# Kernel optimization log

Hardware: AMD Instinct MI355X
Metric: run time of the kernel (lower is better)

Reference implementation:

```python
import jax, jax.numpy as jnp
import numpy as np

B, S, HID = 2, 2048, 3072
H, KV, D = 16, 8, 256
EPS = 1e-6
SCALE = D ** -0.5  # query_pre_attn_scalar is None -> head_dim**-0.5
NEG = -1e9


def setup_inputs() -> dict:
    key = jax.random.key(0)
    ks = jax.random.split(key, 7)
    hidden_states = jax.random.normal(ks[0], (B, S, HID), jnp.float32)
    # rotary tables: freqs_cis = exp(i * pos * theta_j), theta_j = 10000^(-2j/D)
    pos = jnp.arange(S, dtype=jnp.float32)
    inv_freq = 1.0 / (10000.0 ** (jnp.arange(0, D, 2, dtype=jnp.float32) / D))  # [D/2]
    ang = pos[:, None] * inv_freq[None, :]  # [S, D/2]
    freqs_cos = jnp.cos(ang)
    freqs_sin = jnp.sin(ang)
    # additive causal mask [1,1,S,S]
    causal = jnp.tril(jnp.ones((S, S), dtype=bool))
    mask = jnp.where(causal, 0.0, NEG).astype(jnp.float32)[None, None]
    q_w = jax.random.normal(ks[1], (HID, H * D), jnp.float32) * 0.02
    k_w = jax.random.normal(ks[2], (HID, KV * D), jnp.float32) * 0.02
    v_w = jax.random.normal(ks[3], (HID, KV * D), jnp.float32) * 0.02
    o_w = jax.random.normal(ks[4], (H * D, HID), jnp.float32) * 0.02
    qnorm_w = jax.random.normal(ks[5], (D,), jnp.float32) * 0.1
    knorm_w = jax.random.normal(ks[6], (D,), jnp.float32) * 0.1
    return dict(hidden_states=hidden_states, freqs_cos=freqs_cos, freqs_sin=freqs_sin,
                mask=mask, q_w=q_w, k_w=k_w, v_w=v_w, o_w=o_w,
                qnorm_w=qnorm_w, knorm_w=knorm_w)


def rmsnorm(x, w, eps=EPS):
    # RMSNorm with add_unit_offset: x * rsqrt(mean(x^2)+eps) * (1 + w)
    x32 = x.astype(jnp.float32)
    n = x32 * jax.lax.rsqrt(jnp.mean(x32 * x32, axis=-1, keepdims=True) + eps)
    return (n * (1.0 + w.astype(jnp.float32))).astype(x.dtype)


def rope(x, cos, sin):
    # x: [B, S, Hx, D]; complex mult with (x1 + i x2), then concat(real, imag)
    x1, x2 = jnp.split(x, 2, axis=-1)  # each [B,S,Hx,D/2]
    c = cos[None, :, None, :]
    s = sin[None, :, None, :]
    return jnp.concatenate([x1 * c - x2 * s, x1 * s + x2 * c], axis=-1)


def reference(hidden_states, freqs_cos, freqs_sin, mask, q_w, k_w, v_w, o_w, qnorm_w, knorm_w):
    bsz, seqlen = hidden_states.shape[0], hidden_states.shape[1]
    xq = (hidden_states @ q_w).reshape(bsz, seqlen, H, D)
    xk = (hidden_states @ k_w).reshape(bsz, seqlen, KV, D)
    xv = (hidden_states @ v_w).reshape(bsz, seqlen, KV, D)
    # QK-norm (use_qk_norm=True)
    xq = rmsnorm(xq, qnorm_w)
    xk = rmsnorm(xk, knorm_w)
    # rotary embeddings
    xq = rope(xq, freqs_cos, freqs_sin)
    xk = rope(xk, freqs_cos, freqs_sin)
    # GQA: repeat kv heads to match query heads
    rep = H // KV
    xk = jnp.repeat(xk, rep, axis=2)
    xv = jnp.repeat(xv, rep, axis=2)
    q = jnp.transpose(xq, (0, 2, 1, 3)) * SCALE  # [B,H,S,D]
    k = jnp.transpose(xk, (0, 2, 1, 3))
    v = jnp.transpose(xv, (0, 2, 1, 3))
    scores = jnp.einsum('bhqd,bhkd->bhqk', q, k) + mask
    probs = jax.nn.softmax(scores.astype(jnp.float32), axis=-1).astype(q.dtype)
    out = jnp.einsum('bhqk,bhkd->bhqd', probs, v)
    out = jnp.transpose(out, (0, 2, 1, 3)).reshape(bsz, seqlen, H * D)
    return out @ o_w
```

## Files before the change

### kernel.cpp

```cpp
#include <hip/hip_runtime.h>
#include <hip/hip_bf16.h>
#include <cstdint>

#define B_   2
#define S_   2048
#define HID_ 3072
#define H_   16
#define KV_  8
#define D_   256
#define HD_  4096
#define KVD_ 2048
#define QKS_ 8192

constexpr float EPS_   = 1e-6f;
constexpr float SCALE_ = 0.0625f;

typedef unsigned short u16;
typedef __attribute__((ext_vector_type(8))) short bf16x8;
typedef __attribute__((ext_vector_type(4))) float f32x4;

__device__ inline float bf2f(u16 u) { return __uint_as_float(((unsigned int)u) << 16); }
__device__ inline u16 f2bf(float f) {
  unsigned int x = __float_as_uint(f);
  x += 0x7fffu + ((x >> 16) & 1u);
  return (u16)(x >> 16);
}

__device__ inline void gll16(const u16* g, u16* l) {
  __builtin_amdgcn_global_load_lds((const __attribute__((address_space(1))) unsigned int*)g,
                                   (__attribute__((address_space(3))) unsigned int*)l,
                                   16, 0, 0);
}

__global__ void cast_f32_bf16(const float* __restrict__ in, u16* __restrict__ out, int n4) {
  int i = blockIdx.x * blockDim.x + threadIdx.x;
  if (i < n4) {
    float4 v = ((const float4*)in)[i];
    ushort4 o;
    o.x = f2bf(v.x); o.y = f2bf(v.y); o.z = f2bf(v.z); o.w = f2bf(v.w);
    ((ushort4*)out)[i] = o;
  }
}

__global__ void transpose_cast(const float* __restrict__ in, u16* __restrict__ out, int K, int N) {
  __shared__ __align__(16) float tile[64][65];
  int n0 = blockIdx.x * 64, k0 = blockIdx.y * 64;
  int t = threadIdx.x;
  int rr = t >> 4, cc = (t & 15) * 4;
  for (int i = 0; i < 4; i++) {
    float4 v = *(const float4*)(&in[(size_t)(k0 + rr + 16 * i) * N + n0 + cc]);
    tile[rr + 16 * i][cc + 0] = v.x; tile[rr + 16 * i][cc + 1] = v.y;
    tile[rr + 16 * i][cc + 2] = v.z; tile[rr + 16 * i][cc + 3] = v.w;
  }
  __syncthreads();
  for (int i = 0; i < 4; i++) {
    int orow = rr + 16 * i;
    ushort4 o;
    o.x = f2bf(tile[cc + 0][orow]); o.y = f2bf(tile[cc + 1][orow]);
    o.z = f2bf(tile[cc + 2][orow]); o.w = f2bf(tile[cc + 3][orow]);
    *(ushort4*)(&out[(size_t)(n0 + orow) * K + k0 + cc]) = o;
  }
}

__global__ void transpose_v(const u16* __restrict__ in, u16* __restrict__ out) {
  __shared__ __align__(16) u16 tile[64][68];
  int n0 = blockIdx.x * 64, tk0 = blockIdx.y * 64;
  int b = tk0 >> 11, s0 = tk0 & (S_ - 1);
  int t = threadIdx.x;
  int rr = t >> 4, cc = (t & 15) * 4;
  for (int i = 0; i < 4; i++) {
    ushort4 v = *(const ushort4*)(&in[(size_t)(tk0 + rr + 16 * i) * QKS_ + n0 + cc]);
    tile[rr + 16 * i][cc + 0] = v.x; tile[rr + 16 * i][cc + 1] = v.y;
    tile[rr + 16 * i][cc + 2] = v.z; tile[rr + 16 * i][cc + 3] = v.w;
  }
  __syncthreads();
  for (int i = 0; i < 4; i++) {
    int orow = rr + 16 * i;
    ushort4 o;
    o.x = tile[cc + 0][orow]; o.y = tile[cc + 1][orow];
    o.z = tile[cc + 2][orow]; o.w = tile[cc + 3][orow];
    *(ushort4*)(&out[((size_t)b << 22) + (size_t)(n0 + orow) * S_ + s0 + cc]) = o;
  }
}

template <bool OUTF32>
__global__ __launch_bounds__(512, 2) void gemm256(const u16* __restrict__ A,
                                                  const u16* __restrict__ Bt,
                                                  void* __restrict__ Cv, int M, int N, int K) {
  __shared__ __align__(16) u16 As[2][16384];
  __shared__ __align__(16) u16 Bs[2][16384];
  int t = threadIdx.x, lane = t & 63, wave = t >> 6;
  int quad = lane >> 4, l16 = lane & 15;
  int wm = wave >> 2, wn = wave & 3;

  int nwg = gridDim.x * gridDim.y;
  int bid = blockIdx.y * gridDim.x + blockIdx.x;
  int sbid = (bid & 7) * (nwg >> 3) + (bid >> 3);
  int bn = (sbid % gridDim.x) * 256;
  int bm = (sbid / gridDim.x) * 256;

  int srow = lane >> 2;
  int scol8 = ((lane & 3) ^ ((lane >> 3) & 3)) * 8;
  const u16* ap = A + (size_t)(bm + srow) * K + scol8;
  const u16* bp = Bt + (size_t)(bn + srow) * K + scol8;
  int nr = (wave & 1) + ((wave >> 1) << 2);

  auto stA = [&](int sr, int sc, int k0, int bufi) {
    gll16(ap + (size_t)(sr * 16) * K + k0 + sc * 32, &As[bufi][(sr * 2 + sc) * 512]);
  };
  auto stB = [&](int sr, int sc, int k0, int bufi) {
    gll16(bp + (size_t)(sr * 16) * K + k0 + sc * 32, &Bs[bufi][(sr * 2 + sc) * 512]);
  };
  auto stageTile = [&](int kt, int bufi) {
    int k0 = kt * 64;
    stA(wave, 0, k0, bufi); stA(wave, 1, k0, bufi);
    stA(wave + 8, 0, k0, bufi); stA(wave + 8, 1, k0, bufi);
    stB(nr, 0, k0, bufi); stB(nr, 1, k0, bufi);
    stB(nr + 2, 0, k0, bufi); stB(nr + 2, 1, k0, bufi);
  };

  int rsw = l16 * 32 + ((quad ^ ((l16 >> 1) & 3)) * 8);
  auto LDA = [&](int bufi, int i, int ks) {
    return *(const bf16x8*)(&As[bufi][((wm * 8 + i) * 2 + ks) * 512 + rsw]);
  };
  auto LDB = [&](int bufi, int j, int ks) {
    return *(const bf16x8*)(&Bs[bufi][((wn * 4 + j) * 2 + ks) * 512 + rsw]);
  };

  f32x4 acc[8][4] = {};
  int NT = K >> 6;

  stageTile(0, 0);
  stageTile(1, 1);
  asm volatile("s_waitcnt vmcnt(8)" ::: "memory");
  __builtin_amdgcn_s_barrier();
  asm volatile("" ::: "memory");

  bf16x8 A0[4][2], A1[4][2], B01[2][2], B23[2][2];
#pragma unroll
  for (int j = 0; j < 2; j++) { B01[j][0] = LDB(0, j, 0); B01[j][1] = LDB(0, j, 1); }
#pragma unroll
  for (int i = 0; i < 4; i++) { A0[i][0] = LDA(0, i, 0); A0[i][1] = LDA(0, i, 1); }

#pragma unroll 1
  for (int kt = 0; kt < NT; kt++) {
    int cur = kt & 1, nxt = cur ^ 1;

#pragma unroll
    for (int i = 0; i < 4; i++) { A1[i][0] = LDA(cur, i + 4, 0); A1[i][1] = LDA(cur, i + 4, 1); }
    asm volatile("s_waitcnt lgkmcnt(8)" ::: "memory");
#pragma unroll
    for (int i = 0; i < 4; i++)
#pragma unroll
      for (int j = 0; j < 2; j++) {
        acc[i][j] = __builtin_amdgcn_mfma_f32_16x16x32_bf16(A0[i][0], B01[j][0], acc[i][j], 0, 0, 0);
        acc[i][j] = __builtin_amdgcn_mfma_f32_16x16x32_bf16(A0[i][1], B01[j][1], acc[i][j], 0, 0, 0);
      }
#pragma unroll
    for (int j = 0; j < 2; j++) { B23[j][0] = LDB(cur, j + 2, 0); B23[j][1] = LDB(cur, j + 2, 1); }
    asm volatile("s_waitcnt lgkmcnt(4)" ::: "memory");
#pragma unroll
    for (int i = 0; i < 4; i++)
#pragma unroll
      for (int j = 0; j < 2; j++) {
        acc[i + 4][j] = __builtin_amdgcn_mfma_f32_16x16x32_bf16(A1[i][0], B01[j][0], acc[i + 4][j], 0, 0, 0);
        acc[i + 4][j] = __builtin_amdgcn_mfma_f32_16x16x32_bf16(A1[i][1], B01[j][1], acc[i + 4][j], 0, 0, 0);
      }
    asm volatile("s_waitcnt lgkmcnt(0)" ::: "memory");
    asm volatile("s_waitcnt vmcnt(0)" ::: "memory");
    __builtin_amdgcn_s_barrier();
    asm volatile("" ::: "memory");
    if (kt + 2 < NT) stageTile(kt + 2, cur);
    __builtin_amdgcn_s_setprio(1);
#pragma unroll
    for (int i = 0; i < 4; i++)
#pragma unroll
      for (int j = 0; j < 2; j++) {
        acc[i][j + 2] = __builtin_amdgcn_mfma_f32_16x16x32_bf16(A0[i][0], B23[j][0], acc[i][j + 2], 0, 0, 0);
        acc[i][j + 2] = __builtin_amdgcn_mfma_f32_16x16x32_bf16(A0[i][1], B23[j][1], acc[i][j + 2], 0, 0, 0);
      }
    __builtin_amdgcn_s_setprio(0);
    if (kt + 1 < NT) {
#pragma unroll
      for (int j = 0; j < 2; j++) { B01[j][0] = LDB(nxt, j, 0); B01[j][1] = LDB(nxt, j, 1); }
    }
    __builtin_amdgcn_s_setprio(1);
#pragma unroll
    for (int i = 0; i < 4; i++)
#pragma unroll
      for (int j = 0; j < 2; j++) {
        acc[i + 4][j + 2] = __builtin_amdgcn_mfma_f32_16x16x32_bf16(A1[i][0], B23[j][0], acc[i + 4][j + 2], 0, 0, 0);
        acc[i + 4][j + 2] = __builtin_amdgcn_mfma_f32_16x16x32_bf16(A1[i][1], B23[j][1], acc[i + 4][j + 2], 0, 0, 0);
      }
    __builtin_amdgcn_s_setprio(0);
    if (kt + 1 < NT) {
#pragma unroll
      for (int i = 0; i < 4; i++) { A0[i][0] = LDA(nxt, i, 0); A0[i][1] = LDA(nxt, i, 1); }
    }
  }

#pragma unroll
  for (int i = 0; i < 8; i++)
#pragma unroll
    for (int j = 0; j < 4; j++)
#pragma unroll
      for (int r = 0; r < 4; r++) {
        int row = bm + wm * 128 + i * 16 + quad * 4 + r;
        int col = bn + wn * 64 + j * 16 + l16;
        float v = acc[i][j][r];
        if (OUTF32) ((float*)Cv)[(size_t)row * N + col] = v;
        else ((u16*)Cv)[(size_t)row * N + col] = f2bf(v);
      }
}

__global__ void rmsnorm_rope(u16* __restrict__ x, const float* __restrict__ w,
                             const float* __restrict__ fc, const float* __restrict__ fsn,
                             int nh, int stride, float outscale) {
  int token = blockIdx.x;
  int head = blockIdx.y * 4 + (threadIdx.x >> 6);
  if (head >= nh) return;
  int lane = threadIdx.x & 63;
  int s = token & (S_ - 1);
  u16* p = x + (size_t)token * stride + head * D_;
  float v0 = bf2f(p[lane]);
  float v1 = bf2f(p[lane + 64]);
  float v2 = bf2f(p[lane + 128]);
  float v3 = bf2f(p[lane + 192]);
  float ss = v0 * v0 + v1 * v1 + v2 * v2 + v3 * v3;
  for (int off = 32; off; off >>= 1) ss += __shfl_xor(ss, off, 64);
  float rs = rsqrtf(ss * (1.0f / D_) + EPS_);
  float n0 = v0 * rs * (1.0f + w[lane]);
  float n1 = v1 * rs * (1.0f + w[lane + 64]);
  float n2 = v2 * rs * (1.0f + w[lane + 128]);
  float n3 = v3 * rs * (1.0f + w[lane + 192]);
  float c0 = fc[s * 128 + lane], s0 = fsn[s * 128 + lane];
  float c1 = fc[s * 128 + lane + 64], s1 = fsn[s * 128 + lane + 64];
  p[lane]       = f2bf((n0 * c0 - n2 * s0) * outscale);
  p[lane + 128] = f2bf((n0 * s0 + n2 * c0) * outscale);
  p[lane + 64]  = f2bf((n1 * c1 - n3 * s1) * outscale);
  p[lane + 192] = f2bf((n1 * s1 + n3 * c1) * outscale);
}

__global__ __launch_bounds__(256, 3) void flash_attn(const u16* __restrict__ Q,
                                                     const u16* __restrict__ Kb,
                                                     const u16* __restrict__ Vt,
                                                     u16* __restrict__ O) {
  __shared__ __align__(16) u16 Ks[2][8 * 1024];
  __shared__ __align__(16) u16 Vs[8 * 1024];
  int t = threadIdx.x, lane = t & 63, wave = t >> 6;
  int quad = lane >> 4, l16 = lane & 15;
  int h = blockIdx.y, b = blockIdx.z;
  int kvh = h >> 1;

  int swz = ((lane & 3) ^ ((lane >> 2) & 3)) * 8;
  int rswz = (quad ^ (l16 & 3)) * 8;
  const u16* kst = Kb + (size_t)(b * S_ + (lane >> 2)) * QKS_ + kvh * D_ + wave * 64 + swz;
  const u16* vst = Vt + ((size_t)b << 22) + (size_t)(kvh * D_ + wave * 64 + (lane >> 2)) * S_ + swz;

  auto stageK = [&](int kt, int bufi) {
    u16* kdst = &Ks[bufi][wave * 2048];
    const u16* ksrc = kst + (size_t)(kt * 32) * QKS_;
#pragma unroll
    for (int c2 = 0; c2 < 2; c2++)
#pragma unroll
      for (int r = 0; r < 2; r++)
        gll16(ksrc + (size_t)(r * 16) * QKS_ + c2 * 32, kdst + c2 * 1024 + r * 512);
  };
  auto stageV = [&](int kt) {
    u16* vdst = &Vs[wave * 2048];
#pragma unroll
    for (int c = 0; c < 4; c++)
      gll16(vst + (size_t)(c * 16) * S_ + kt * 32, vdst + c * 512);
  };

#pragma unroll 1
  for (int half = 0; half < 2; half++) {
    int qb = (half == 0) ? (31 - (int)blockIdx.x) * 64 : (int)blockIdx.x * 64;
    int qw = qb + wave * 16;

    bf16x8 qf[8];
    const u16* qp = Q + ((size_t)(b * S_) + qw + l16) * QKS_ + h * D_;
#pragma unroll
    for (int c = 0; c < 8; c++) qf[c] = *(const bf16x8*)(qp + c * 32 + quad * 8);

    f32x4 o_acc[16] = {};
    float m_s = -3e38f, l_s = 0.f;

    int nkt = (qb + 64) >> 5;
    stageK(0, 0);
    stageV(0);
#pragma unroll 1
    for (int kt = 0; kt < nkt; kt++) {
      int cur = kt & 1;
      asm volatile("s_waitcnt vmcnt(4)" ::: "memory");
      __builtin_amdgcn_s_barrier();
      asm volatile("" ::: "memory");
      if (kt + 1 < nkt) stageK(kt + 1, cur ^ 1);

      f32x4 sc0 = {}, sc1 = {};
#pragma unroll
      for (int c = 0; c < 8; c++) {
        bf16x8 k0 = *(const bf16x8*)(&Ks[cur][c * 1024 + l16 * 32 + rswz]);
        bf16x8 k1 = *(const bf16x8*)(&Ks[cur][c * 1024 + (l16 + 16) * 32 + rswz]);
        sc0 = __builtin_amdgcn_mfma_f32_16x16x32_bf16(k0, qf[c], sc0, 0, 0, 0);
        sc1 = __builtin_amdgcn_mfma_f32_16x16x32_bf16(k1, qf[c], sc1, 0, 0, 0);
      }

      int qg = qw + l16;
      int kbase = kt * 32 + quad * 4;
      float p0[4], p1[4];
      float mx = -1e30f;
#pragma unroll
      for (int r = 0; r < 4; r++) {
        p0[r] = (kbase + r <= qg) ? sc0[r] : -1e30f;
        p1[r] = (kbase + 16 + r <= qg) ? sc1[r] : -1e30f;
        mx = fmaxf(mx, fmaxf(p0[r], p1[r]));
      }
      mx = fmaxf(mx, __shfl_xor(mx, 16));
      mx = fmaxf(mx, __shfl_xor(mx, 32));
      float mn = fmaxf(m_s, mx);
      bool chg = mn > m_s;
      float rsum = 0.f;
#pragma unroll
      for (int r = 0; r < 4; r++) {
        p0[r] = __expf(p0[r] - mn);
        p1[r] = __expf(p1[r] - mn);
        rsum += p0[r] + p1[r];
      }
      if (__any((int)chg)) {
        float alpha = __expf(m_s - mn);
        float ar[4];
#pragma unroll
        for (int r = 0; r < 4; r++) ar[r] = __shfl(alpha, quad * 20 + r);
#pragma unroll
        for (int nt = 0; nt < 16; nt++)
#pragma unroll
          for (int r = 0; r < 4; r++) o_acc[nt][r] *= ar[r];
        l_s *= alpha;
      }
      m_s = mn;
      rsum += __shfl_xor(rsum, 16);
      rsum += __shfl_xor(rsum, 32);
      l_s += rsum;

      unsigned int w_[4], x_[4], gl[4], gh[4], sn[4], rc[4];
      w_[0] = (unsigned)f2bf(p0[0]) | ((unsigned)f2bf(p0[1]) << 16);
      w_[1] = (unsigned)f2bf(p0[2]) | ((unsigned)f2bf(p0[3]) << 16);
      w_[2] = (unsigned)f2bf(p1[0]) | ((unsigned)f2bf(p1[1]) << 16);
      w_[3] = (unsigned)f2bf(p1[2]) | ((unsigned)f2bf(p1[3]) << 16);
#pragma unroll
      for (int i = 0; i < 4; i++) x_[i] = (unsigned)__shfl_xor((int)w_[i], 16);
      bool odd = (quad & 1) != 0;
      gl[0] = odd ? x_[0] : w_[0]; gl[1] = odd ? x_[1] : w_[1];
      gl[2] = odd ? w_[0] : x_[0]; gl[3] = odd ? w_[1] : x_[1];
      gh[0] = odd ? x_[2] : w_[2]; gh[1] = odd ? x_[3] : w_[3];
      gh[2] = odd ? w_[2] : x_[2]; gh[3] = odd ? w_[3] : x_[3];
#pragma unroll
      for (int i = 0; i < 4; i++) sn[i] = odd ? gl[i] : gh[i];
#pragma unroll
      for (int i = 0; i < 4; i++) rc[i] = (unsigned)__shfl_xor((int)sn[i], 32);
      union { unsigned int u[4]; bf16x8 v; } pfc;
#pragma unroll
      for (int i = 0; i < 4; i++)
        pfc.u[i] = (quad == 0) ? gl[i] : (quad == 3) ? gh[i] : rc[i];
      bf16x8 pf = pfc.v;

      if (kt + 1 < nkt) asm volatile("s_waitcnt vmcnt(4)" ::: "memory");
      else              asm volatile("s_waitcnt vmcnt(0)" ::: "memory");
      __builtin_amdgcn_s_barrier();
      asm volatile("" ::: "memory");

#pragma unroll
      for (int nt = 0; nt < 16; nt++) {
        bf16x8 vf = *(const bf16x8*)(&Vs[(nt * 16 + l16) * 32 + rswz]);
        o_acc[nt] = __builtin_amdgcn_mfma_f32_16x16x32_bf16(pf, vf, o_acc[nt], 0, 0, 0);
      }

      asm volatile("s_waitcnt lgkmcnt(0)" ::: "memory");
      __builtin_amdgcn_s_barrier();
      asm volatile("" ::: "memory");
      if (kt + 1 < nkt) stageV(kt + 1);
    }

    float invl = 1.0f / l_s;
    float inv_r[4];
#pragma unroll
    for (int r = 0; r < 4; r++) inv_r[r] = __shfl(invl, quad * 20 + r);
    for (int r = 0; r < 4; r++) {
      int qg2 = qw + quad * 4 + r;
      u16* op = O + ((size_t)(b * S_) + qg2) * HD_ + h * D_;
      for (int nt = 0; nt < 16; nt++) op[nt * 16 + l16] = f2bf(o_acc[nt][r] * inv_r[r]);
    }
  }
}

extern "C" void kernel_launch(void* const* d_in, const int* in_sizes, int n_in,
                              void* d_out, int out_size, void* d_ws, size_t ws_size,
                              hipStream_t stream) {
  const float* hs  = (const float*)d_in[0];
  const float* fc  = (const float*)d_in[1];
  const float* fsn = (const float*)d_in[2];
  const float* qw  = (const float*)d_in[4];
  const float* kw  = (const float*)d_in[5];
  const float* vw  = (const float*)d_in[6];
  const float* ow  = (const float*)d_in[7];
  const float* qnw = (const float*)d_in[8];
  const float* knw = (const float*)d_in[9];

  char* ws = (char*)d_ws;
  u16* x_bf   = (u16*)(ws + 0);
  u16* vt     = (u16*)(ws + 0);
  u16* wqkv_t = (u16*)(ws + 25165824);
  u16* kw_t   = (u16*)(ws + 50331648);
  u16* vw_t   = (u16*)(ws + 62914560);
  u16* ow_t   = (u16*)(ws + 75497472);
  u16* xqkv   = (u16*)(ws + 100663296);
  u16* attn   = (u16*)(ws + 25165824);

  cast_f32_bf16<<<12288, 256, 0, stream>>>(hs, x_bf, 4096 * 3072 / 4);
  transpose_cast<<<dim3(64, 48), 256, 0, stream>>>(qw, wqkv_t, 3072, 4096);
  transpose_cast<<<dim3(32, 48), 256, 0, stream>>>(kw, kw_t, 3072, 2048);
  transpose_cast<<<dim3(32, 48), 256, 0, stream>>>(vw, vw_t, 3072, 2048);
  transpose_cast<<<dim3(48, 64), 256, 0, stream>>>(ow, ow_t, 4096, 3072);

  gemm256<false><<<dim3(32, 16), 512, 0, stream>>>(x_bf, wqkv_t, xqkv, 4096, 8192, 3072);

  rmsnorm_rope<<<dim3(4096, 4), 256, 0, stream>>>(xqkv, qnw, fc, fsn, 16, QKS_, SCALE_);
  rmsnorm_rope<<<dim3(4096, 2), 256, 0, stream>>>(xqkv + 4096, knw, fc, fsn, 8, QKS_, 1.0f);

  transpose_v<<<dim3(32, 64), 256, 0, stream>>>(xqkv + 6144, vt);

  flash_attn<<<dim3(16, 16, 2), 256, 0, stream>>>(xqkv, xqkv + 4096, vt, attn);

  gemm256<true><<<dim3(12, 16), 512, 0, stream>>>(attn, ow_t, (float*)d_out, 4096, 3072, 4096);
}
```

Measured before the change: 747.1 us.

## Load GEMM B operand directly from global into registers, bypassing LDS

The B tile is no longer staged through shared memory. Each wave now loads its B fragments straight from global memory into registers one k-tile ahead, and only A stays double-buffered in LDS. This halves LDS usage and removes the B LDS writes and reads plus part of the staging traffic. In exchange, each B element is fetched from global/L2 by both row-waves of the block, the global loads are less coalesced, and the vmcnt waits become more fragile.

```diff
diff --git a/kernel.cpp b/kernel.cpp
--- a/kernel.cpp
+++ b/kernel.cpp
@@ -88,7 +88,6 @@
                                                   const u16* __restrict__ Bt,
                                                   void* __restrict__ Cv, int M, int N, int K) {
   __shared__ __align__(16) u16 As[2][16384];
-  __shared__ __align__(16) u16 Bs[2][16384];
   int t = threadIdx.x, lane = t & 63, wave = t >> 6;
   int quad = lane >> 4, l16 = lane & 15;
   int wm = wave >> 2, wn = wave & 3;
@@ -102,53 +101,53 @@
   int srow = lane >> 2;
   int scol8 = ((lane & 3) ^ ((lane >> 3) & 3)) * 8;
   const u16* ap = A + (size_t)(bm + srow) * K + scol8;
-  const u16* bp = Bt + (size_t)(bn + srow) * K + scol8;
-  int nr = (wave & 1) + ((wave >> 1) << 2);
 
   auto stA = [&](int sr, int sc, int k0, int bufi) {
     gll16(ap + (size_t)(sr * 16) * K + k0 + sc * 32, &As[bufi][(sr * 2 + sc) * 512]);
   };
-  auto stB = [&](int sr, int sc, int k0, int bufi) {
-    gll16(bp + (size_t)(sr * 16) * K + k0 + sc * 32, &Bs[bufi][(sr * 2 + sc) * 512]);
-  };
-  auto stageTile = [&](int kt, int bufi) {
+  auto stageTileA = [&](int kt, int bufi) {
     int k0 = kt * 64;
-    stA(wave, 0, k0, bufi); stA(wave, 1, k0, bufi);
-    stA(wave + 8, 0, k0, bufi); stA(wave + 8, 1, k0, bufi);
-    stB(nr, 0, k0, bufi); stB(nr, 1, k0, bufi);
-    stB(nr + 2, 0, k0, bufi); stB(nr + 2, 1, k0, bufi);
+    stA(wave * 2, 0, k0, bufi); stA(wave * 2, 1, k0, bufi);
+    stA(wave * 2 + 1, 0, k0, bufi); stA(wave * 2 + 1, 1, k0, bufi);
   };
 
   int rsw = l16 * 32 + ((quad ^ ((l16 >> 1) & 3)) * 8);
   auto LDA = [&](int bufi, int i, int ks) {
     return *(const bf16x8*)(&As[bufi][((wm * 8 + i) * 2 + ks) * 512 + rsw]);
   };
-  auto LDB = [&](int bufi, int j, int ks) {
-    return *(const bf16x8*)(&Bs[bufi][((wn * 4 + j) * 2 + ks) * 512 + rsw]);
+
+  const u16* bq = Bt + (size_t)(bn + wn * 64 + l16) * K + quad * 8;
+  auto GLB = [&](int j, int ks, int kt2) {
+    return *(const bf16x8*)(bq + (size_t)(j * 16) * K + kt2 * 64 + ks * 32);
   };
 
   f32x4 acc[8][4] = {};
   int NT = K >> 6;
 
-  stageTile(0, 0);
-  stageTile(1, 1);
-  asm volatile("s_waitcnt vmcnt(8)" ::: "memory");
+  bf16x8 A0[4][2], A1[4][2], B01[2][2], B23[2][2];
+
+  stageTileA(0, 0);
+  stageTileA(1, 1);
+#pragma unroll
+  for (int j = 0; j < 2; j++) { B01[j][0] = GLB(j, 0, 0); B01[j][1] = GLB(j, 1, 0); }
+#pragma unroll
+  for (int j = 0; j < 2; j++) { B23[j][0] = GLB(j + 2, 0, 0); B23[j][1] = GLB(j + 2, 1, 0); }
+  asm volatile("s_waitcnt vmcnt(12)" ::: "memory");
   __builtin_amdgcn_s_barrier();
   asm volatile("" ::: "memory");
-
-  bf16x8 A0[4][2], A1[4][2], B01[2][2], B23[2][2];
-#pragma unroll
-  for (int j = 0; j < 2; j++) { B01[j][0] = LDB(0, j, 0); B01[j][1] = LDB(0, j, 1); }
 #pragma unroll
   for (int i = 0; i < 4; i++) { A0[i][0] = LDA(0, i, 0); A0[i][1] = LDA(0, i, 1); }
 
 #pragma unroll 1
   for (int kt = 0; kt < NT; kt++) {
     int cur = kt & 1, nxt = cur ^ 1;
+    bool rd = (kt + 1) < NT;
 
 #pragma unroll
     for (int i = 0; i < 4; i++) { A1[i][0] = LDA(cur, i + 4, 0); A1[i][1] = LDA(cur, i + 4, 1); }
     asm volatile("s_waitcnt lgkmcnt(8)" ::: "memory");
+    asm volatile("s_waitcnt vmcnt(4)" ::: "memory");
+    __builtin_amdgcn_s_setprio(1);
 #pragma unroll
     for (int i = 0; i < 4; i++)
 #pragma unroll
@@ -156,9 +155,9 @@
         acc[i][j] = __builtin_amdgcn_mfma_f32_16x16x32_bf16(A0[i][0], B01[j][0], acc[i][j], 0, 0, 0);
         acc[i][j] = __builtin_amdgcn_mfma_f32_16x16x32_bf16(A0[i][1], B01[j][1], acc[i][j], 0, 0, 0);
       }
-#pragma unroll
-    for (int j = 0; j < 2; j++) { B23[j][0] = LDB(cur, j + 2, 0); B23[j][1] = LDB(cur, j + 2, 1); }
-    asm volatile("s_waitcnt lgkmcnt(4)" ::: "memory");
+    __builtin_amdgcn_s_setprio(0);
+    asm volatile("s_waitcnt lgkmcnt(0)" ::: "memory");
+    __builtin_amdgcn_s_setprio(1);
 #pragma unroll
     for (int i = 0; i < 4; i++)
 #pragma unroll
@@ -166,11 +165,11 @@
         acc[i + 4][j] = __builtin_amdgcn_mfma_f32_16x16x32_bf16(A1[i][0], B01[j][0], acc[i + 4][j], 0, 0, 0);
         acc[i + 4][j] = __builtin_amdgcn_mfma_f32_16x16x32_bf16(A1[i][1], B01[j][1], acc[i + 4][j], 0, 0, 0);
       }
-    asm volatile("s_waitcnt lgkmcnt(0)" ::: "memory");
+    __builtin_amdgcn_s_setprio(0);
     asm volatile("s_waitcnt vmcnt(0)" ::: "memory");
     __builtin_amdgcn_s_barrier();
     asm volatile("" ::: "memory");
-    if (kt + 2 < NT) stageTile(kt + 2, cur);
+    if (kt + 2 < NT) stageTileA(kt + 2, cur);
     __builtin_amdgcn_s_setprio(1);
 #pragma unroll
     for (int i = 0; i < 4; i++)
@@ -180,9 +179,9 @@
         acc[i][j + 2] = __builtin_amdgcn_mfma_f32_16x16x32_bf16(A0[i][1], B23[j][1], acc[i][j + 2], 0, 0, 0);
       }
     __builtin_amdgcn_s_setprio(0);
-    if (kt + 1 < NT) {
-#pragma unroll
-      for (int j = 0; j < 2; j++) { B01[j][0] = LDB(nxt, j, 0); B01[j][1] = LDB(nxt, j, 1); }
+    if (rd) {
+#pragma unroll
+      for (int j = 0; j < 2; j++) { B01[j][0] = GLB(j, 0, kt + 1); B01[j][1] = GLB(j, 1, kt + 1); }
     }
     __builtin_amdgcn_s_setprio(1);
 #pragma unroll
@@ -193,7 +192,11 @@
         acc[i + 4][j + 2] = __builtin_amdgcn_mfma_f32_16x16x32_bf16(A1[i][1], B23[j][1], acc[i + 4][j + 2], 0, 0, 0);
       }
     __builtin_amdgcn_s_setprio(0);
-    if (kt + 1 < NT) {
+    if (rd) {
+#pragma unroll
+      for (int j = 0; j < 2; j++) { B23[j][0] = GLB(j + 2, 0, kt + 1); B23[j][1] = GLB(j + 2, 1, kt + 1); }
+    }
+    if (rd) {
 #pragma unroll
       for (int i = 0; i < 4; i++) { A0[i][0] = LDA(nxt, i, 0); A0[i][1] = LDA(nxt, i, 1); }
     }
```

After: 908.6 us. 1.22x slower.

## Restructure GEMM main loop into 8-phase schedule with interleaved half-tile prefetch

Applied to the files above, without the earlier changes.

Replaces the per-k-tile double-buffered GEMM loop with a two-tile unrolled, eight-phase schedule. Global-to-LDS loads for A and B halves are spread across the MFMA clusters, each cluster is bracketed by barriers, and LDS reads are issued between clusters. The aim is to overlap global loads, LDS reads and MFMA more evenly and shorten stalls at the single big barrier. In exchange it adds many more barriers per iteration and relies on careful vmcnt accounting and on K/64 being even.

```diff
diff --git a/kernel.cpp b/kernel.cpp
--- a/kernel.cpp
+++ b/kernel.cpp
@@ -103,7 +103,6 @@
   int scol8 = ((lane & 3) ^ ((lane >> 3) & 3)) * 8;
   const u16* ap = A + (size_t)(bm + srow) * K + scol8;
   const u16* bp = Bt + (size_t)(bn + srow) * K + scol8;
-  int nr = (wave & 1) + ((wave >> 1) << 2);
 
   auto stA = [&](int sr, int sc, int k0, int bufi) {
     gll16(ap + (size_t)(sr * 16) * K + k0 + sc * 32, &As[bufi][(sr * 2 + sc) * 512]);
@@ -111,12 +110,13 @@
   auto stB = [&](int sr, int sc, int k0, int bufi) {
     gll16(bp + (size_t)(sr * 16) * K + k0 + sc * 32, &Bs[bufi][(sr * 2 + sc) * 512]);
   };
-  auto stageTile = [&](int kt, int bufi) {
-    int k0 = kt * 64;
-    stA(wave, 0, k0, bufi); stA(wave, 1, k0, bufi);
-    stA(wave + 8, 0, k0, bufi); stA(wave + 8, 1, k0, bufi);
-    stB(nr, 0, k0, bufi); stB(nr, 1, k0, bufi);
-    stB(nr + 2, 0, k0, bufi); stB(nr + 2, 1, k0, bufi);
+  auto stAh = [&](int h, int kt, int bufi) {
+    stA(h * 8 + wave, 0, kt * 64, bufi);
+    stA(h * 8 + wave, 1, kt * 64, bufi);
+  };
+  auto stBh = [&](int h, int kt, int bufi) {
+    stB(h * 8 + wave, 0, kt * 64, bufi);
+    stB(h * 8 + wave, 1, kt * 64, bufi);
   };
 
   int rsw = l16 * 32 + ((quad ^ ((l16 >> 1) & 3)) * 8);
@@ -128,76 +128,92 @@
   };
 
   f32x4 acc[8][4] = {};
-  int NT = K >> 6;
-
-  stageTile(0, 0);
-  stageTile(1, 1);
-  asm volatile("s_waitcnt vmcnt(8)" ::: "memory");
+  bf16x8 A0[4][2], A1[4][2], B01[2][2], B23[2][2];
+  int NT = K >> 6, NP = NT >> 1;
+
+  stAh(0, 0, 0); stAh(1, 0, 0);
+  stBh(0, 0, 0); stBh(1, 0, 0);
+  stAh(0, 1, 1); stAh(1, 1, 1);
+  asm volatile("s_waitcnt vmcnt(4)" ::: "memory");
   __builtin_amdgcn_s_barrier();
   asm volatile("" ::: "memory");
-
-  bf16x8 A0[4][2], A1[4][2], B01[2][2], B23[2][2];
 #pragma unroll
   for (int j = 0; j < 2; j++) { B01[j][0] = LDB(0, j, 0); B01[j][1] = LDB(0, j, 1); }
-#pragma unroll
-  for (int i = 0; i < 4; i++) { A0[i][0] = LDA(0, i, 0); A0[i][1] = LDA(0, i, 1); }
+
+#define MFMA_CL(IOFS, JOFS, AA, BB)                                            \
+  __builtin_amdgcn_s_setprio(1);                                               \
+  _Pragma("unroll")                                                            \
+  for (int i_ = 0; i_ < 4; i_++)                                               \
+    _Pragma("unroll")                                                          \
+    for (int j_ = 0; j_ < 2; j_++) {                                           \
+      acc[i_ + IOFS][j_ + JOFS] = __builtin_amdgcn_mfma_f32_16x16x32_bf16(     \
+          AA[i_][0], BB[j_][0], acc[i_ + IOFS][j_ + JOFS], 0, 0, 0);           \
+      acc[i_ + IOFS][j_ + JOFS] = __builtin_amdgcn_mfma_f32_16x16x32_bf16(     \
+          AA[i_][1], BB[j_][1], acc[i_ + IOFS][j_ + JOFS], 0, 0, 0);           \
+    }                                                                          \
+  __builtin_amdgcn_s_setprio(0);
+
+#define PH_TAIL(IOFS, JOFS, AA, BB)                                            \
+  __builtin_amdgcn_s_barrier();                                                \
+  asm volatile("s_waitcnt lgkmcnt(0)" ::: "memory");                           \
+  MFMA_CL(IOFS, JOFS, AA, BB)                                                  \
+  __builtin_amdgcn_s_barrier();                                                \
+  asm volatile("" ::: "memory");
 
 #pragma unroll 1
-  for (int kt = 0; kt < NT; kt++) {
-    int cur = kt & 1, nxt = cur ^ 1;
-
-#pragma unroll
-    for (int i = 0; i < 4; i++) { A1[i][0] = LDA(cur, i + 4, 0); A1[i][1] = LDA(cur, i + 4, 1); }
-    asm volatile("s_waitcnt lgkmcnt(8)" ::: "memory");
-#pragma unroll
-    for (int i = 0; i < 4; i++)
-#pragma unroll
-      for (int j = 0; j < 2; j++) {
-        acc[i][j] = __builtin_amdgcn_mfma_f32_16x16x32_bf16(A0[i][0], B01[j][0], acc[i][j], 0, 0, 0);
-        acc[i][j] = __builtin_amdgcn_mfma_f32_16x16x32_bf16(A0[i][1], B01[j][1], acc[i][j], 0, 0, 0);
-      }
-#pragma unroll
-    for (int j = 0; j < 2; j++) { B23[j][0] = LDB(cur, j + 2, 0); B23[j][1] = LDB(cur, j + 2, 1); }
-    asm volatile("s_waitcnt lgkmcnt(4)" ::: "memory");
-#pragma unroll
-    for (int i = 0; i < 4; i++)
-#pragma unroll
-      for (int j = 0; j < 2; j++) {
-        acc[i + 4][j] = __builtin_amdgcn_mfma_f32_16x16x32_bf16(A1[i][0], B01[j][0], acc[i + 4][j], 0, 0, 0);
-        acc[i + 4][j] = __builtin_amdgcn_mfma_f32_16x16x32_bf16(A1[i][1], B01[j][1], acc[i + 4][j], 0, 0, 0);
-      }
+  for (int u = 0; u < NP; u++) {
+    bool sL = (u + 1) < NP;
+    int k2 = 2 * u + 2, k3 = 2 * u + 3;
+
+#pragma unroll
+    for (int i = 0; i < 4; i++) { A0[i][0] = LDA(0, i, 0); A0[i][1] = LDA(0, i, 1); }
+    stBh(0, 2 * u + 1, 1);
+    PH_TAIL(0, 0, A0, B01)
+#pragma unroll
+    for (int i = 0; i < 4; i++) { A1[i][0] = LDA(0, i + 4, 0); A1[i][1] = LDA(0, i + 4, 1); }
+    stBh(1, 2 * u + 1, 1);
+    PH_TAIL(4, 0, A1, B01)
+#pragma unroll
+    for (int j = 0; j < 2; j++) { B23[j][0] = LDB(0, j + 2, 0); B23[j][1] = LDB(0, j + 2, 1); }
+    if (sL) stAh(0, k2, 0);
+    PH_TAIL(0, 2, A0, B23)
+    if (sL) asm volatile("s_waitcnt vmcnt(2)" ::: "memory");
+    else    asm volatile("s_waitcnt vmcnt(0)" ::: "memory");
+    if (sL) stAh(1, k2, 0);
+    __builtin_amdgcn_s_barrier();
     asm volatile("s_waitcnt lgkmcnt(0)" ::: "memory");
-    asm volatile("s_waitcnt vmcnt(0)" ::: "memory");
+    MFMA_CL(4, 2, A1, B23)
+#pragma unroll
+    for (int j = 0; j < 2; j++) { B01[j][0] = LDB(1, j, 0); B01[j][1] = LDB(1, j, 1); }
     __builtin_amdgcn_s_barrier();
     asm volatile("" ::: "memory");
-    if (kt + 2 < NT) stageTile(kt + 2, cur);
-    __builtin_amdgcn_s_setprio(1);
-#pragma unroll
-    for (int i = 0; i < 4; i++)
-#pragma unroll
-      for (int j = 0; j < 2; j++) {
-        acc[i][j + 2] = __builtin_amdgcn_mfma_f32_16x16x32_bf16(A0[i][0], B23[j][0], acc[i][j + 2], 0, 0, 0);
-        acc[i][j + 2] = __builtin_amdgcn_mfma_f32_16x16x32_bf16(A0[i][1], B23[j][1], acc[i][j + 2], 0, 0, 0);
-      }
-    __builtin_amdgcn_s_setprio(0);
-    if (kt + 1 < NT) {
-#pragma unroll
-      for (int j = 0; j < 2; j++) { B01[j][0] = LDB(nxt, j, 0); B01[j][1] = LDB(nxt, j, 1); }
+#pragma unroll
+    for (int i = 0; i < 4; i++) { A0[i][0] = LDA(1, i, 0); A0[i][1] = LDA(1, i, 1); }
+    if (sL) stBh(0, k2, 0);
+    PH_TAIL(0, 0, A0, B01)
+#pragma unroll
+    for (int i = 0; i < 4; i++) { A1[i][0] = LDA(1, i + 4, 0); A1[i][1] = LDA(1, i + 4, 1); }
+    if (sL) stBh(1, k2, 0);
+    PH_TAIL(4, 0, A1, B01)
+#pragma unroll
+    for (int j = 0; j < 2; j++) { B23[j][0] = LDB(1, j + 2, 0); B23[j][1] = LDB(1, j + 2, 1); }
+    if (sL) stAh(0, k3, 1);
+    PH_TAIL(0, 2, A0, B23)
+    if (sL) asm volatile("s_waitcnt vmcnt(2)" ::: "memory");
+    else    asm volatile("s_waitcnt vmcnt(0)" ::: "memory");
+    if (sL) stAh(1, k3, 1);
+    __builtin_amdgcn_s_barrier();
+    asm volatile("s_waitcnt lgkmcnt(0)" ::: "memory");
+    MFMA_CL(4, 2, A1, B23)
+    if (sL) {
+#pragma unroll
+      for (int j = 0; j < 2; j++) { B01[j][0] = LDB(0, j, 0); B01[j][1] = LDB(0, j, 1); }
     }
-    __builtin_amdgcn_s_setprio(1);
-#pragma unroll
-    for (int i = 0; i < 4; i++)
-#pragma unroll
-      for (int j = 0; j < 2; j++) {
-        acc[i + 4][j + 2] = __builtin_amdgcn_mfma_f32_16x16x32_bf16(A1[i][0], B23[j][0], acc[i + 4][j + 2], 0, 0, 0);
-        acc[i + 4][j + 2] = __builtin_amdgcn_mfma_f32_16x16x32_bf16(A1[i][1], B23[j][1], acc[i + 4][j + 2], 0, 0, 0);
-      }
-    __builtin_amdgcn_s_setprio(0);
-    if (kt + 1 < NT) {
-#pragma unroll
-      for (int i = 0; i < 4; i++) { A0[i][0] = LDA(nxt, i, 0); A0[i][1] = LDA(nxt, i, 1); }
-    }
-  }
+    __builtin_amdgcn_s_barrier();
+    asm volatile("" ::: "memory");
+  }
+#undef PH_TAIL
+#undef MFMA_CL
 
 #pragma unroll
   for (int i = 0; i < 8; i++)
```

Measured after the change: 788.1 us. 1.05x slower.

## Merge prep and post-QKV kernels; give each attention wave two query tiles

Applied to the files above, without the earlier changes.

Folds the cast and four weight transpose-casts into one prep kernel, and the Q/K rmsnorm-rope plus V transpose into one post_qkv kernel, removing several launches. Flash attention drops to 2 waves per block, with each wave handling 32 query rows as two 16-row groups. Each K/V fragment read from LDS now feeds two MFMAs, and each wave stages twice as much K/V. The trade is more accumulator registers per wave (o_acc doubles) and fewer waves per block, which may lower occupancy and latency hiding.

```diff
diff --git a/kernel.cpp b/kernel.cpp
--- a/kernel.cpp
+++ b/kernel.cpp
@@ -32,20 +32,10 @@
                                    16, 0, 0);
 }
 
-__global__ void cast_f32_bf16(const float* __restrict__ in, u16* __restrict__ out, int n4) {
-  int i = blockIdx.x * blockDim.x + threadIdx.x;
-  if (i < n4) {
-    float4 v = ((const float4*)in)[i];
-    ushort4 o;
-    o.x = f2bf(v.x); o.y = f2bf(v.y); o.z = f2bf(v.z); o.w = f2bf(v.w);
-    ((ushort4*)out)[i] = o;
-  }
-}
-
-__global__ void transpose_cast(const float* __restrict__ in, u16* __restrict__ out, int K, int N) {
+__device__ inline void tc_tile(const float* __restrict__ in, u16* __restrict__ out,
+                               int K, int N, int bx, int by, int t) {
   __shared__ __align__(16) float tile[64][65];
-  int n0 = blockIdx.x * 64, k0 = blockIdx.y * 64;
-  int t = threadIdx.x;
+  int n0 = bx * 64, k0 = by * 64;
   int rr = t >> 4, cc = (t & 15) * 4;
   for (int i = 0; i < 4; i++) {
     float4 v = *(const float4*)(&in[(size_t)(k0 + rr + 16 * i) * N + n0 + cc]);
@@ -62,24 +52,29 @@
   }
 }
 
-__global__ void transpose_v(const u16* __restrict__ in, u16* __restrict__ out) {
-  __shared__ __align__(16) u16 tile[64][68];
-  int n0 = blockIdx.x * 64, tk0 = blockIdx.y * 64;
-  int b = tk0 >> 11, s0 = tk0 & (S_ - 1);
-  int t = threadIdx.x;
-  int rr = t >> 4, cc = (t & 15) * 4;
-  for (int i = 0; i < 4; i++) {
-    ushort4 v = *(const ushort4*)(&in[(size_t)(tk0 + rr + 16 * i) * QKS_ + n0 + cc]);
-    tile[rr + 16 * i][cc + 0] = v.x; tile[rr + 16 * i][cc + 1] = v.y;
-    tile[rr + 16 * i][cc + 2] = v.z; tile[rr + 16 * i][cc + 3] = v.w;
-  }
-  __syncthreads();
-  for (int i = 0; i < 4; i++) {
-    int orow = rr + 16 * i;
+__global__ void prep(const float* __restrict__ hs, u16* __restrict__ x_bf,
+                     const float* __restrict__ qw, const float* __restrict__ kw,
+                     const float* __restrict__ vw, const float* __restrict__ ow,
+                     u16* __restrict__ wqkv_t, u16* __restrict__ ow_t) {
+  int bid = blockIdx.x, t = threadIdx.x;
+  if (bid < 12288) {
+    int i = bid * 256 + t;
+    float4 v = ((const float4*)hs)[i];
     ushort4 o;
-    o.x = tile[cc + 0][orow]; o.y = tile[cc + 1][orow];
-    o.z = tile[cc + 2][orow]; o.w = tile[cc + 3][orow];
-    *(ushort4*)(&out[((size_t)b << 22) + (size_t)(n0 + orow) * S_ + s0 + cc]) = o;
+    o.x = f2bf(v.x); o.y = f2bf(v.y); o.z = f2bf(v.z); o.w = f2bf(v.w);
+    ((ushort4*)x_bf)[i] = o;
+  } else if (bid < 15360) {
+    int r = bid - 12288;
+    tc_tile(qw, wqkv_t, 3072, 4096, r % 64, r / 64, t);
+  } else if (bid < 16896) {
+    int r = bid - 15360;
+    tc_tile(kw, wqkv_t + (size_t)4096 * 3072, 3072, 2048, r % 32, r / 32, t);
+  } else if (bid < 18432) {
+    int r = bid - 16896;
+    tc_tile(vw, wqkv_t + (size_t)6144 * 3072, 3072, 2048, r % 32, r / 32, t);
+  } else {
+    int r = bid - 18432;
+    tc_tile(ow, ow_t, 4096, 3072, r % 48, r / 48, t);
   }
 }
 
@@ -213,35 +208,62 @@
       }
 }
 
-__global__ void rmsnorm_rope(u16* __restrict__ x, const float* __restrict__ w,
-                             const float* __restrict__ fc, const float* __restrict__ fsn,
-                             int nh, int stride, float outscale) {
-  int token = blockIdx.x;
-  int head = blockIdx.y * 4 + (threadIdx.x >> 6);
-  if (head >= nh) return;
-  int lane = threadIdx.x & 63;
-  int s = token & (S_ - 1);
-  u16* p = x + (size_t)token * stride + head * D_;
-  float v0 = bf2f(p[lane]);
-  float v1 = bf2f(p[lane + 64]);
-  float v2 = bf2f(p[lane + 128]);
-  float v3 = bf2f(p[lane + 192]);
-  float ss = v0 * v0 + v1 * v1 + v2 * v2 + v3 * v3;
-  for (int off = 32; off; off >>= 1) ss += __shfl_xor(ss, off, 64);
-  float rs = rsqrtf(ss * (1.0f / D_) + EPS_);
-  float n0 = v0 * rs * (1.0f + w[lane]);
-  float n1 = v1 * rs * (1.0f + w[lane + 64]);
-  float n2 = v2 * rs * (1.0f + w[lane + 128]);
-  float n3 = v3 * rs * (1.0f + w[lane + 192]);
-  float c0 = fc[s * 128 + lane], s0 = fsn[s * 128 + lane];
-  float c1 = fc[s * 128 + lane + 64], s1 = fsn[s * 128 + lane + 64];
-  p[lane]       = f2bf((n0 * c0 - n2 * s0) * outscale);
-  p[lane + 128] = f2bf((n0 * s0 + n2 * c0) * outscale);
-  p[lane + 64]  = f2bf((n1 * c1 - n3 * s1) * outscale);
-  p[lane + 192] = f2bf((n1 * s1 + n3 * c1) * outscale);
-}
-
-__global__ __launch_bounds__(256, 3) void flash_attn(const u16* __restrict__ Q,
+__global__ void post_qkv(u16* __restrict__ xqkv, const float* __restrict__ qnw,
+                         const float* __restrict__ knw, const float* __restrict__ fc,
+                         const float* __restrict__ fsn, u16* __restrict__ vt) {
+  int bid = blockIdx.x, t = threadIdx.x;
+  if (bid < 24576) {
+    int token = bid & 4095, y = bid >> 12;
+    int lane = t & 63;
+    const float* w;
+    u16* p;
+    float outscale;
+    if (y < 4) { w = qnw; outscale = SCALE_;
+      p = xqkv + (size_t)token * QKS_ + (y * 4 + (t >> 6)) * D_; }
+    else { w = knw; outscale = 1.0f;
+      p = xqkv + 4096 + (size_t)token * QKS_ + ((y - 4) * 4 + (t >> 6)) * D_; }
+    int s = token & (S_ - 1);
+    float v0 = bf2f(p[lane]);
+    float v1 = bf2f(p[lane + 64]);
+    float v2 = bf2f(p[lane + 128]);
+    float v3 = bf2f(p[lane + 192]);
+    float ss = v0 * v0 + v1 * v1 + v2 * v2 + v3 * v3;
+    for (int off = 32; off; off >>= 1) ss += __shfl_xor(ss, off, 64);
+    float rs = rsqrtf(ss * (1.0f / D_) + EPS_);
+    float n0 = v0 * rs * (1.0f + w[lane]);
+    float n1 = v1 * rs * (1.0f + w[lane + 64]);
+    float n2 = v2 * rs * (1.0f + w[lane + 128]);
+    float n3 = v3 * rs * (1.0f + w[lane + 192]);
+    float c0 = fc[s * 128 + lane], s0 = fsn[s * 128 + lane];
+    float c1 = fc[s * 128 + lane + 64], s1 = fsn[s * 128 + lane + 64];
+    p[lane]       = f2bf((n0 * c0 - n2 * s0) * outscale);
+    p[lane + 128] = f2bf((n0 * s0 + n2 * c0) * outscale);
+    p[lane + 64]  = f2bf((n1 * c1 - n3 * s1) * outscale);
+    p[lane + 192] = f2bf((n1 * s1 + n3 * c1) * outscale);
+  } else {
+    __shared__ __align__(16) u16 tile[64][68];
+    int r = bid - 24576;
+    int n0 = (r & 31) * 64, tk0 = (r >> 5) * 64;
+    int b = tk0 >> 11, s0 = tk0 & (S_ - 1);
+    int rr = t >> 4, cc = (t & 15) * 4;
+    const u16* in = xqkv + 6144;
+    for (int i = 0; i < 4; i++) {
+      ushort4 v = *(const ushort4*)(&in[(size_t)(tk0 + rr + 16 * i) * QKS_ + n0 + cc]);
+      tile[rr + 16 * i][cc + 0] = v.x; tile[rr + 16 * i][cc + 1] = v.y;
+      tile[rr + 16 * i][cc + 2] = v.z; tile[rr + 16 * i][cc + 3] = v.w;
+    }
+    __syncthreads();
+    for (int i = 0; i < 4; i++) {
+      int orow = rr + 16 * i;
+      ushort4 o;
+      o.x = tile[cc + 0][orow]; o.y = tile[cc + 1][orow];
+      o.z = tile[cc + 2][orow]; o.w = tile[cc + 3][orow];
+      *(ushort4*)(&vt[((size_t)b << 22) + (size_t)(n0 + orow) * S_ + s0 + cc]) = o;
+    }
+  }
+}
+
+__global__ __launch_bounds__(128, 2) void flash_attn(const u16* __restrict__ Q,
                                                      const u16* __restrict__ Kb,
                                                      const u16* __restrict__ Vt,
                                                      u16* __restrict__ O) {
@@ -254,37 +276,40 @@
 
   int swz = ((lane & 3) ^ ((lane >> 2) & 3)) * 8;
   int rswz = (quad ^ (l16 & 3)) * 8;
-  const u16* kst = Kb + (size_t)(b * S_ + (lane >> 2)) * QKS_ + kvh * D_ + wave * 64 + swz;
-  const u16* vst = Vt + ((size_t)b << 22) + (size_t)(kvh * D_ + wave * 64 + (lane >> 2)) * S_ + swz;
+  const u16* kst = Kb + (size_t)(b * S_ + (lane >> 2)) * QKS_ + kvh * D_ + wave * 128 + swz;
+  const u16* vst = Vt + ((size_t)b << 22) + (size_t)(kvh * D_ + wave * 128 + (lane >> 2)) * S_ + swz;
 
   auto stageK = [&](int kt, int bufi) {
-    u16* kdst = &Ks[bufi][wave * 2048];
+    u16* kdst = &Ks[bufi][wave * 4096];
     const u16* ksrc = kst + (size_t)(kt * 32) * QKS_;
 #pragma unroll
-    for (int c2 = 0; c2 < 2; c2++)
+    for (int c2 = 0; c2 < 4; c2++)
 #pragma unroll
       for (int r = 0; r < 2; r++)
         gll16(ksrc + (size_t)(r * 16) * QKS_ + c2 * 32, kdst + c2 * 1024 + r * 512);
   };
   auto stageV = [&](int kt) {
-    u16* vdst = &Vs[wave * 2048];
-#pragma unroll
-    for (int c = 0; c < 4; c++)
+    u16* vdst = &Vs[wave * 4096];
+#pragma unroll
+    for (int c = 0; c < 8; c++)
       gll16(vst + (size_t)(c * 16) * S_ + kt * 32, vdst + c * 512);
   };
 
 #pragma unroll 1
   for (int half = 0; half < 2; half++) {
     int qb = (half == 0) ? (31 - (int)blockIdx.x) * 64 : (int)blockIdx.x * 64;
-    int qw = qb + wave * 16;
-
-    bf16x8 qf[8];
-    const u16* qp = Q + ((size_t)(b * S_) + qw + l16) * QKS_ + h * D_;
-#pragma unroll
-    for (int c = 0; c < 8; c++) qf[c] = *(const bf16x8*)(qp + c * 32 + quad * 8);
-
-    f32x4 o_acc[16] = {};
-    float m_s = -3e38f, l_s = 0.f;
+    int qw = qb + wave * 32;
+
+    bf16x8 qf[2][8];
+#pragma unroll
+    for (int g = 0; g < 2; g++) {
+      const u16* qp = Q + ((size_t)(b * S_) + qw + g * 16 + l16) * QKS_ + h * D_;
+#pragma unroll
+      for (int c = 0; c < 8; c++) qf[g][c] = *(const bf16x8*)(qp + c * 32 + quad * 8);
+    }
+
+    f32x4 o_acc[2][16] = {};
+    float m_s[2] = {-3e38f, -3e38f}, l_s[2] = {0.f, 0.f};
 
     int nkt = (qb + 64) >> 5;
     stageK(0, 0);
@@ -292,80 +317,86 @@
 #pragma unroll 1
     for (int kt = 0; kt < nkt; kt++) {
       int cur = kt & 1;
-      asm volatile("s_waitcnt vmcnt(4)" ::: "memory");
+      asm volatile("s_waitcnt vmcnt(8)" ::: "memory");
       __builtin_amdgcn_s_barrier();
       asm volatile("" ::: "memory");
       if (kt + 1 < nkt) stageK(kt + 1, cur ^ 1);
 
-      f32x4 sc0 = {}, sc1 = {};
+      f32x4 sc[2][2] = {};
 #pragma unroll
       for (int c = 0; c < 8; c++) {
         bf16x8 k0 = *(const bf16x8*)(&Ks[cur][c * 1024 + l16 * 32 + rswz]);
         bf16x8 k1 = *(const bf16x8*)(&Ks[cur][c * 1024 + (l16 + 16) * 32 + rswz]);
-        sc0 = __builtin_amdgcn_mfma_f32_16x16x32_bf16(k0, qf[c], sc0, 0, 0, 0);
-        sc1 = __builtin_amdgcn_mfma_f32_16x16x32_bf16(k1, qf[c], sc1, 0, 0, 0);
-      }
-
-      int qg = qw + l16;
-      int kbase = kt * 32 + quad * 4;
-      float p0[4], p1[4];
-      float mx = -1e30f;
-#pragma unroll
-      for (int r = 0; r < 4; r++) {
-        p0[r] = (kbase + r <= qg) ? sc0[r] : -1e30f;
-        p1[r] = (kbase + 16 + r <= qg) ? sc1[r] : -1e30f;
-        mx = fmaxf(mx, fmaxf(p0[r], p1[r]));
-      }
-      mx = fmaxf(mx, __shfl_xor(mx, 16));
-      mx = fmaxf(mx, __shfl_xor(mx, 32));
-      float mn = fmaxf(m_s, mx);
-      bool chg = mn > m_s;
-      float rsum = 0.f;
-#pragma unroll
-      for (int r = 0; r < 4; r++) {
-        p0[r] = __expf(p0[r] - mn);
-        p1[r] = __expf(p1[r] - mn);
-        rsum += p0[r] + p1[r];
-      }
-      if (__any((int)chg)) {
-        float alpha = __expf(m_s - mn);
-        float ar[4];
-#pragma unroll
-        for (int r = 0; r < 4; r++) ar[r] = __shfl(alpha, quad * 20 + r);
-#pragma unroll
-        for (int nt = 0; nt < 16; nt++)
-#pragma unroll
-          for (int r = 0; r < 4; r++) o_acc[nt][r] *= ar[r];
-        l_s *= alpha;
-      }
-      m_s = mn;
-      rsum += __shfl_xor(rsum, 16);
-      rsum += __shfl_xor(rsum, 32);
-      l_s += rsum;
-
-      unsigned int w_[4], x_[4], gl[4], gh[4], sn[4], rc[4];
-      w_[0] = (unsigned)f2bf(p0[0]) | ((unsigned)f2bf(p0[1]) << 16);
-      w_[1] = (unsigned)f2bf(p0[2]) | ((unsigned)f2bf(p0[3]) << 16);
-      w_[2] = (unsigned)f2bf(p1[0]) | ((unsigned)f2bf(p1[1]) << 16);
-      w_[3] = (unsigned)f2bf(p1[2]) | ((unsigned)f2bf(p1[3]) << 16);
-#pragma unroll
-      for (int i = 0; i < 4; i++) x_[i] = (unsigned)__shfl_xor((int)w_[i], 16);
-      bool odd = (quad & 1) != 0;
-      gl[0] = odd ? x_[0] : w_[0]; gl[1] = odd ? x_[1] : w_[1];
-      gl[2] = odd ? w_[0] : x_[0]; gl[3] = odd ? w_[1] : x_[1];
-      gh[0] = odd ? x_[2] : w_[2]; gh[1] = odd ? x_[3] : w_[3];
-      gh[2] = odd ? w_[2] : x_[2]; gh[3] = odd ? w_[3] : x_[3];
-#pragma unroll
-      for (int i = 0; i < 4; i++) sn[i] = odd ? gl[i] : gh[i];
-#pragma unroll
-      for (int i = 0; i < 4; i++) rc[i] = (unsigned)__shfl_xor((int)sn[i], 32);
-      union { unsigned int u[4]; bf16x8 v; } pfc;
-#pragma unroll
-      for (int i = 0; i < 4; i++)
-        pfc.u[i] = (quad == 0) ? gl[i] : (quad == 3) ? gh[i] : rc[i];
-      bf16x8 pf = pfc.v;
-
-      if (kt + 1 < nkt) asm volatile("s_waitcnt vmcnt(4)" ::: "memory");
+        sc[0][0] = __builtin_amdgcn_mfma_f32_16x16x32_bf16(k0, qf[0][c], sc[0][0], 0, 0, 0);
+        sc[0][1] = __builtin_amdgcn_mfma_f32_16x16x32_bf16(k1, qf[0][c], sc[0][1], 0, 0, 0);
+        sc[1][0] = __builtin_amdgcn_mfma_f32_16x16x32_bf16(k0, qf[1][c], sc[1][0], 0, 0, 0);
+        sc[1][1] = __builtin_amdgcn_mfma_f32_16x16x32_bf16(k1, qf[1][c], sc[1][1], 0, 0, 0);
+      }
+
+      bf16x8 pf[2];
+#pragma unroll
+      for (int g = 0; g < 2; g++) {
+        int qg = qw + g * 16 + l16;
+        int kbase = kt * 32 + quad * 4;
+        float p0[4], p1[4];
+        float mx = -1e30f;
+#pragma unroll
+        for (int r = 0; r < 4; r++) {
+          p0[r] = (kbase + r <= qg) ? sc[g][0][r] : -1e30f;
+          p1[r] = (kbase + 16 + r <= qg) ? sc[g][1][r] : -1e30f;
+          mx = fmaxf(mx, fmaxf(p0[r], p1[r]));
+        }
+        mx = fmaxf(mx, __shfl_xor(mx, 16));
+        mx = fmaxf(mx, __shfl_xor(mx, 32));
+        float mn = fmaxf(m_s[g], mx);
+        bool chg = mn > m_s[g];
+        float rsum = 0.f;
+#pragma unroll
+        for (int r = 0; r < 4; r++) {
+          p0[r] = __expf(p0[r] - mn);
+          p1[r] = __expf(p1[r] - mn);
+          rsum += p0[r] + p1[r];
+        }
+        if (__any((int)chg)) {
+          float alpha = __expf(m_s[g] - mn);
+          float ar[4];
+#pragma unroll
+          for (int r = 0; r < 4; r++) ar[r] = __shfl(alpha, quad * 20 + r);
+#pragma unroll
+          for (int nt = 0; nt < 16; nt++)
+#pragma unroll
+            for (int r = 0; r < 4; r++) o_acc[g][nt][r] *= ar[r];
+          l_s[g] *= alpha;
+        }
+        m_s[g] = mn;
+        rsum += __shfl_xor(rsum, 16);
+        rsum += __shfl_xor(rsum, 32);
+        l_s[g] += rsum;
+
+        unsigned int w_[4], x_[4], gl[4], gh[4], sn[4], rc[4];
+        w_[0] = (unsigned)f2bf(p0[0]) | ((unsigned)f2bf(p0[1]) << 16);
+        w_[1] = (unsigned)f2bf(p0[2]) | ((unsigned)f2bf(p0[3]) << 16);
+        w_[2] = (unsigned)f2bf(p1[0]) | ((unsigned)f2bf(p1[1]) << 16);
+        w_[3] = (unsigned)f2bf(p1[2]) | ((unsigned)f2bf(p1[3]) << 16);
+#pragma unroll
+        for (int i = 0; i < 4; i++) x_[i] = (unsigned)__shfl_xor((int)w_[i], 16);
+        bool odd = (quad & 1) != 0;
+        gl[0] = odd ? x_[0] : w_[0]; gl[1] = odd ? x_[1] : w_[1];
+        gl[2] = odd ? w_[0] : x_[0]; gl[3] = odd ? w_[1] : x_[1];
+        gh[0] = odd ? x_[2] : w_[2]; gh[1] = odd ? x_[3] : w_[3];
+        gh[2] = odd ? w_[2] : x_[2]; gh[3] = odd ? w_[3] : x_[3];
+#pragma unroll
+        for (int i = 0; i < 4; i++) sn[i] = odd ? gl[i] : gh[i];
+#pragma unroll
+        for (int i = 0; i < 4; i++) rc[i] = (unsigned)__shfl_xor((int)sn[i], 32);
+        union { unsigned int u[4]; bf16x8 v; } pfc;
+#pragma unroll
+        for (int i = 0; i < 4; i++)
+          pfc.u[i] = (quad == 0) ? gl[i] : (quad == 3) ? gh[i] : rc[i];
+        pf[g] = pfc.v;
+      }
+
+      if (kt + 1 < nkt) asm volatile("s_waitcnt vmcnt(8)" ::: "memory");
       else              asm volatile("s_waitcnt vmcnt(0)" ::: "memory");
       __builtin_amdgcn_s_barrier();
       asm volatile("" ::: "memory");
@@ -373,7 +404,8 @@
 #pragma unroll
       for (int nt = 0; nt < 16; nt++) {
         bf16x8 vf = *(const bf16x8*)(&Vs[(nt * 16 + l16) * 32 + rswz]);
-        o_acc[nt] = __builtin_amdgcn_mfma_f32_16x16x32_bf16(pf, vf, o_acc[nt], 0, 0, 0);
+        o_acc[0][nt] = __builtin_amdgcn_mfma_f32_16x16x32_bf16(pf[0], vf, o_acc[0][nt], 0, 0, 0);
+        o_acc[1][nt] = __builtin_amdgcn_mfma_f32_16x16x32_bf16(pf[1], vf, o_acc[1][nt], 0, 0, 0);
       }
 
       asm volatile("s_waitcnt lgkmcnt(0)" ::: "memory");
@@ -382,14 +414,17 @@
       if (kt + 1 < nkt) stageV(kt + 1);
     }
 
-    float invl = 1.0f / l_s;
-    float inv_r[4];
-#pragma unroll
-    for (int r = 0; r < 4; r++) inv_r[r] = __shfl(invl, quad * 20 + r);
-    for (int r = 0; r < 4; r++) {
-      int qg2 = qw + quad * 4 + r;
-      u16* op = O + ((size_t)(b * S_) + qg2) * HD_ + h * D_;
-      for (int nt = 0; nt < 16; nt++) op[nt * 16 + l16] = f2bf(o_acc[nt][r] * inv_r[r]);
+#pragma unroll
+    for (int g = 0; g < 2; g++) {
+      float invl = 1.0f / l_s[g];
+      float inv_r[4];
+#pragma unroll
+      for (int r = 0; r < 4; r++) inv_r[r] = __shfl(invl, quad * 20 + r);
+      for (int r = 0; r < 4; r++) {
+        int qg2 = qw + g * 16 + quad * 4 + r;
+        u16* op = O + ((size_t)(b * S_) + qg2) * HD_ + h * D_;
+        for (int nt = 0; nt < 16; nt++) op[nt * 16 + l16] = f2bf(o_acc[g][nt][r] * inv_r[r]);
+      }
     }
   }
 }
@@ -411,26 +446,17 @@
   u16* x_bf   = (u16*)(ws + 0);
   u16* vt     = (u16*)(ws + 0);
   u16* wqkv_t = (u16*)(ws + 25165824);
-  u16* kw_t   = (u16*)(ws + 50331648);
-  u16* vw_t   = (u16*)(ws + 62914560);
   u16* ow_t   = (u16*)(ws + 75497472);
   u16* xqkv   = (u16*)(ws + 100663296);
   u16* attn   = (u16*)(ws + 25165824);
 
-  cast_f32_bf16<<<12288, 256, 0, stream>>>(hs, x_bf, 4096 * 3072 / 4);
-  transpose_cast<<<dim3(64, 48), 256, 0, stream>>>(qw, wqkv_t, 3072, 4096);
-  transpose_cast<<<dim3(32, 48), 256, 0, stream>>>(kw, kw_t, 3072, 2048);
-  transpose_cast<<<dim3(32, 48), 256, 0, stream>>>(vw, vw_t, 3072, 2048);
-  transpose_cast<<<dim3(48, 64), 256, 0, stream>>>(ow, ow_t, 4096, 3072);
+  prep<<<21504, 256, 0, stream>>>(hs, x_bf, qw, kw, vw, ow, wqkv_t, ow_t);
 
   gemm256<false><<<dim3(32, 16), 512, 0, stream>>>(x_bf, wqkv_t, xqkv, 4096, 8192, 3072);
 
-  rmsnorm_rope<<<dim3(4096, 4), 256, 0, stream>>>(xqkv, qnw, fc, fsn, 16, QKS_, SCALE_);
-  rmsnorm_rope<<<dim3(4096, 2), 256, 0, stream>>>(xqkv + 4096, knw, fc, fsn, 8, QKS_, 1.0f);
-
-  transpose_v<<<dim3(32, 64), 256, 0, stream>>>(xqkv + 6144, vt);
-
-  flash_attn<<<dim3(16, 16, 2), 256, 0, stream>>>(xqkv, xqkv + 4096, vt, attn);
+  post_qkv<<<26624, 256, 0, stream>>>(xqkv, qnw, knw, fc, fsn, vt);
+
+  flash_attn<<<dim3(16, 16, 2), 128, 0, stream>>>(xqkv, xqkv + 4096, vt, attn);
 
   gemm256<true><<<dim3(12, 16), 512, 0, stream>>>(attn, ow_t, (float*)d_out, 4096, 3072, 4096);
 }
```

Result: slower. 807.6 us (+8.1%).
